# Kernel optimization log

Measured on AMD Instinct MI355X. Metric: run time of the kernel, lower is better.

The kernel has to match this reference:

```python
import jax, jax.numpy as jnp
import numpy as np

N = 50000          # nodes
E = 800000         # edges (avg degree 16)
D = 128            # feature dim
MSG_EPS = 1e-7     # GENConv eps added to relu(msg)
SM_EPS = 1e-16     # pyg softmax denominator eps
BN_EPS = 1e-5
LN_EPS = 1e-5


def setup_inputs() -> dict:
    key = jax.random.key(0)
    ks = jax.random.split(key, 6)
    x = jax.random.normal(ks[0], (N, D), dtype=jnp.float32)
    edge_index = jax.random.randint(ks[1], (2, E), 0, N, dtype=jnp.int32)
    t = jnp.array(1.0, dtype=jnp.float32)
    W1 = jax.random.normal(ks[2], (D, 2 * D), dtype=jnp.float32) / np.sqrt(D).astype(np.float32)
    b1 = jnp.zeros((2 * D,), jnp.float32)
    bn_gamma = jnp.ones((2 * D,), jnp.float32)
    bn_beta = jnp.zeros((2 * D,), jnp.float32)
    W2 = jax.random.normal(ks[3], (2 * D, D), dtype=jnp.float32) / np.sqrt(2 * D).astype(np.float32)
    b2 = jnp.zeros((D,), jnp.float32)
    ln_gamma = jnp.ones((D,), jnp.float32)
    ln_beta = jnp.zeros((D,), jnp.float32)
    return {"x": x, "edge_index": edge_index, "t": t, "W1": W1, "b1": b1,
            "bn_gamma": bn_gamma, "bn_beta": bn_beta, "W2": W2, "b2": b2,
            "ln_gamma": ln_gamma, "ln_beta": ln_beta}


def reference(x, edge_index, t, W1, b1, bn_gamma, bn_beta, W2, b2, ln_gamma, ln_beta):
    src, dst = edge_index[0], edge_index[1]
    # --- GENConv message: relu(x_j) + eps  -> [E, D]
    msg = jax.nn.relu(x[src]) + MSG_EPS
    # --- softmax aggregation over incoming edges per dst node, per feature
    logits = t * msg                                            # [E, D]
    seg_max = jax.ops.segment_max(logits, dst, num_segments=N)  # [N, D]
    seg_max = jnp.where(jnp.isfinite(seg_max), seg_max, 0.0)    # empty segments -> 0
    ex = jnp.exp(logits - seg_max[dst])                         # [E, D]
    denom = jax.ops.segment_sum(ex, dst, num_segments=N)        # [N, D]
    alpha = ex / (denom[dst] + SM_EPS)                          # [E, D]
    agg = jax.ops.segment_sum(alpha * msg, dst, num_segments=N) # [N, D]
    # --- GENConv update: MLP(agg + x), MLP = Lin(D,2D)->BN->ReLU->Lin(2D,D)
    h = agg + x
    h = h @ W1 + b1                                             # [N, 2D]
    mu = jnp.mean(h, axis=0)
    var = jnp.var(h, axis=0)
    h = (h - mu) * jax.lax.rsqrt(var + BN_EPS) * bn_gamma + bn_beta
    h = jax.nn.relu(h)
    h = h @ W2 + b2                                             # [N, D]
    # --- LayerNorm -> ReLU -> (dropout p=0 noop) -> residual
    mu2 = jnp.mean(h, axis=-1, keepdims=True)
    var2 = jnp.mean(jnp.square(h - mu2), axis=-1, keepdims=True)
    h = (h - mu2) * jax.lax.rsqrt(var2 + LN_EPS) * ln_gamma + ln_beta
    h = jax.nn.relu(h)
    return x + h
```

## Files before the change

### kernel.cpp

```cpp
#include <hip/hip_runtime.h>

#define D 128
#define D2 256
#define BSH 5
#define BNODES 32
#define NBMAX 2048
#define CAP 640
#define PCHUNK 4096
#define REP 32
#define CSTRIDE 16
#define ZWORDS (2 * REP * 256 + NBMAX * CSTRIDE)

typedef __attribute__((ext_vector_type(8))) short short8;
typedef __attribute__((ext_vector_type(4))) float f32x4;

__device__ inline unsigned short f2b(float f) {
  unsigned u = __float_as_uint(f);
  unsigned r = (u + 0x7FFFu + ((u >> 16) & 1u)) >> 16;
  return (unsigned short)r;
}
__device__ inline float b2f(unsigned short h) {
  return __uint_as_float(((unsigned)h) << 16);
}
__device__ inline float lo2f(unsigned u) { return __uint_as_float(u << 16); }
__device__ inline float hi2f(unsigned u) { return __uint_as_float(u & 0xffff0000u); }

__global__ __launch_bounds__(256) void prep_kernel(
    const float* __restrict__ x, const float* __restrict__ W1,
    const float* __restrict__ W2, unsigned short* __restrict__ mb,
    unsigned short* __restrict__ W1f, unsigned short* __restrict__ W2f,
    float* __restrict__ zbase, int total4) {
  int idx = blockIdx.x * 256 + threadIdx.x;
  if (idx < 32768) {
    int k = idx >> 8, n = idx & 255;
    int t = n >> 4, m16 = n & 15;
    int kk = k >> 5, quad = (k >> 3) & 3, j = k & 7;
    W1f[(((t * 4 + kk) * 64 + quad * 16 + m16) << 3) + j] = f2b(W1[idx]);
  } else if (idx < 65536) {
    int i = idx - 32768;
    int k = i >> 7, n = i & 127;
    int t = n >> 4, m16 = n & 15;
    int kk = k >> 5, quad = (k >> 3) & 3, j = k & 7;
    W2f[(((t * 8 + kk) * 64 + quad * 16 + m16) << 3) + j] = f2b(W2[i]);
  } else if (idx < 65536 + total4) {
    int i = idx - 65536;
    float4 v = reinterpret_cast<const float4*>(x)[i];
    unsigned lo = (unsigned)f2b(fmaxf(v.x, 0.f) + 1e-7f) |
                  ((unsigned)f2b(fmaxf(v.y, 0.f) + 1e-7f) << 16);
    unsigned hi = (unsigned)f2b(fmaxf(v.z, 0.f) + 1e-7f) |
                  ((unsigned)f2b(fmaxf(v.w, 0.f) + 1e-7f) << 16);
    reinterpret_cast<uint2*>(mb)[i] = make_uint2(lo, hi);
  } else if (idx < 65536 + total4 + 32) {
    reinterpret_cast<uint2*>(mb)[idx - 65536] = make_uint2(0u, 0u);
  } else if (idx < 65536 + total4 + 32 + ZWORDS) {
    zbase[idx - (65536 + total4 + 32)] = 0.f;
  }
}

__global__ __launch_bounds__(256) void part_kernel(const int* __restrict__ ei,
                                                   int* __restrict__ cursor,
                                                   unsigned* __restrict__ pairbuf,
                                                   int E, int nb) {
  __shared__ int cnt[NBMAX];
  __shared__ int base[NBMAX];
  int tid = threadIdx.x;
  int c0 = blockIdx.x * PCHUNK;
  int nE = min(PCHUNK, E - c0);
  for (int i = tid; i < nb; i += 256) cnt[i] = 0;
  __syncthreads();
  for (int j = tid; j < nE; j += 256) {
    int dst = ei[E + c0 + j];
    atomicAdd(&cnt[dst >> BSH], 1);
  }
  __syncthreads();
  for (int i = tid; i < nb; i += 256) {
    int c = cnt[i];
    base[i] = (c > 0) ? atomicAdd(&cursor[i * CSTRIDE], c) : 0;
    cnt[i] = 0;
  }
  __syncthreads();
  for (int j = tid; j < nE; j += 256) {
    int e = c0 + j;
    int dst = ei[E + e];
    int src = ei[e];
    int b = dst >> BSH;
    int r = base[b] + atomicAdd(&cnt[b], 1);
    if (r < CAP)
      pairbuf[(size_t)b * CAP + r] =
          (unsigned)src | ((unsigned)(dst & (BNODES - 1)) << 16);
  }
}

__global__ __launch_bounds__(512) void agg2_kernel(const float* __restrict__ x,
                                                   const unsigned short* __restrict__ mb,
                                                   const unsigned* __restrict__ pairbuf,
                                                   const int* __restrict__ cursor,
                                                   const float* __restrict__ tptr,
                                                   unsigned short* __restrict__ h0b, int N) {
  __shared__ int soff[CAP + 4 * BNODES];
  __shared__ int cnt[BNODES], off[BNODES], run[BNODES], pcnt[BNODES];
  int b = blockIdx.x;
  int tid = threadIdx.x;
  int Eb = min(cursor[b * CSTRIDE], CAP);
  if (tid < BNODES) { cnt[tid] = 0; run[tid] = 0; }
  __syncthreads();
  for (int j = tid; j < Eb; j += 512)
    atomicAdd(&cnt[pairbuf[(size_t)b * CAP + j] >> 16], 1);
  __syncthreads();
  if (tid < BNODES) {
    int c = cnt[tid];
    int pc = (c + 3) & ~3;
    pcnt[tid] = pc;
    int s = pc;
#pragma unroll
    for (int st = 1; st < 32; st <<= 1) {
      int u = __shfl_up(s, st, 32);
      if ((tid & 31) >= st) s += u;
    }
    off[tid] = s - pc;
  }
  __syncthreads();
  for (int j = tid; j < Eb; j += 512) {
    unsigned p = pairbuf[(size_t)b * CAP + j];
    int dl = p >> 16;
    int r = atomicAdd(&run[dl], 1);
    soff[off[dl] + r] = (int)(p & 0xffffu) << 8;
  }
  if (tid < BNODES) {
    int o = off[tid];
    for (int r = cnt[tid]; r < pcnt[tid]; ++r) soff[o + r] = N << 8;
  }
  __syncthreads();

  int w = tid >> 6;
  int l = tid & 63;
  float t = tptr[0];
  int laneoff = l << 2;
  const char* mbase = (const char*)mb;
  for (int ln = w; ln < BNODES; ln += 8) {
    int n = (b << BSH) + ln;
    if (n >= N) continue;
    int s0 = off[ln];
    int dn = pcnt[ln];
    float den0 = 0.f, num0 = 0.f, den1 = 0.f, num1 = 0.f;
    if (dn > 0) {
      unsigned uu[4];
#pragma unroll
      for (int q = 0; q < 4; ++q)
        uu[q] = *(const unsigned*)(mbase + (soff[s0 + q] | laneoff));
      for (int j = 4; j < dn; j += 4) {
        unsigned vv[4];
#pragma unroll
        for (int q = 0; q < 4; ++q)
          vv[q] = *(const unsigned*)(mbase + (soff[s0 + j + q] | laneoff));
#pragma unroll
        for (int q = 0; q < 4; ++q) {
          float m0 = lo2f(uu[q]);
          float m1 = hi2f(uu[q]);
          float e0 = __expf(t * m0);
          float e1 = __expf(t * m1);
          den0 += e0; num0 += e0 * m0;
          den1 += e1; num1 += e1 * m1;
        }
#pragma unroll
        for (int q = 0; q < 4; ++q) uu[q] = vv[q];
      }
#pragma unroll
      for (int q = 0; q < 4; ++q) {
        float m0 = lo2f(uu[q]);
        float m1 = hi2f(uu[q]);
        float e0 = __expf(t * m0);
        float e1 = __expf(t * m1);
        den0 += e0; num0 += e0 * m0;
        den1 += e1; num1 += e1 * m1;
      }
      float fnpad = (float)(dn - cnt[ln]);
      den0 -= fnpad;
      den1 -= fnpad;
    }
    size_t idx = ((size_t)n << 7) + 2 * l;
    float2 xv = *reinterpret_cast<const float2*>(x + idx);
    float v0 = num0 / (den0 + 1e-16f) + xv.x;
    float v1 = num1 / (den1 + 1e-16f) + xv.y;
    *reinterpret_cast<unsigned*>(h0b + idx) =
        (unsigned)f2b(v0) | ((unsigned)f2b(v1) << 16);
  }
}

__global__ __launch_bounds__(256) void gemm1_mfma(
    const unsigned short* __restrict__ h0b, const unsigned short* __restrict__ W1f,
    unsigned short* __restrict__ h1b,
    float* __restrict__ bnsum, float* __restrict__ bnsumsq, int M) {
  __shared__ unsigned short lt[4][64][72];
  int tid = threadIdx.x;
  int w = tid >> 6;
  int l = tid & 63;
  int m16 = l & 15;
  int quad = l >> 4;
  int r0 = blockIdx.x * 64;

  f32x4 acc[4][4];
#pragma unroll
  for (int rt = 0; rt < 4; ++rt)
#pragma unroll
    for (int ct = 0; ct < 4; ++ct) acc[rt][ct] = (f32x4){0.f, 0.f, 0.f, 0.f};

#pragma unroll
  for (int kk = 0; kk < 4; ++kk) {
    short8 bfr[4];
#pragma unroll
    for (int ct = 0; ct < 4; ++ct)
      bfr[ct] = *reinterpret_cast<const short8*>(
          W1f + ((((w * 4 + ct) * 4 + kk) * 64 + l) << 3));
    short8 a[4];
#pragma unroll
    for (int rt = 0; rt < 4; ++rt) {
      int row = min(r0 + rt * 16 + m16, M - 1);
      a[rt] = *reinterpret_cast<const short8*>(h0b + (size_t)row * D + kk * 32 + quad * 8);
    }
#pragma unroll
    for (int rt = 0; rt < 4; ++rt)
#pragma unroll
      for (int ct = 0; ct < 4; ++ct)
        acc[rt][ct] = __builtin_amdgcn_mfma_f32_16x16x32_bf16(a[rt], bfr[ct], acc[rt][ct], 0, 0, 0);
  }

  int rep = (blockIdx.x & (REP - 1)) << 8;
#pragma unroll
  for (int ct = 0; ct < 4; ++ct) {
    int col = w * 64 + ct * 16 + m16;
    float cs = 0.f, cq = 0.f;
#pragma unroll
    for (int rt = 0; rt < 4; ++rt) {
      int rloc = rt * 16 + quad * 4;
#pragma unroll
      for (int reg = 0; reg < 4; ++reg) {
        float val = acc[rt][ct][reg];
        if (r0 + rloc + reg < M) {
          cs += val;
          cq += val * val;
        }
        lt[w][rloc + reg][ct * 16 + m16] = f2b(val);
      }
    }
    cs += __shfl_xor(cs, 16, 64);
    cs += __shfl_xor(cs, 32, 64);
    cq += __shfl_xor(cq, 16, 64);
    cq += __shfl_xor(cq, 32, 64);
    if (quad == 0) {
      atomicAdd(&bnsum[rep + col], cs);
      atomicAdd(&bnsumsq[rep + col], cq);
    }
  }

  int row = r0 + l;
  if (row < M) {
    const unsigned short* src = &lt[w][l][0];
    unsigned short* dst = h1b + (size_t)row * D2 + w * 64;
#pragma unroll
    for (int j = 0; j < 8; ++j)
      *reinterpret_cast<short8*>(dst + j * 8) =
          *reinterpret_cast<const short8*>(src + j * 8);
  }
}

__global__ __launch_bounds__(256) void gemm2_mfma(
    const unsigned short* __restrict__ h1b, const unsigned short* __restrict__ W2f,
    const float* __restrict__ b2, const float* __restrict__ bnsum,
    const float* __restrict__ bnsumsq, const float* __restrict__ bng,
    const float* __restrict__ bnb, const float* __restrict__ lng,
    const float* __restrict__ lnb, const float* __restrict__ x,
    float* __restrict__ out, int M) {
  __shared__ float lnp[64][2], lnp2[64][2];
  __shared__ float sS[D2], sH[D2];
  int tid = threadIdx.x;
  {
    float s = 0.f, q = 0.f;
#pragma unroll
    for (int r = 0; r < REP; ++r) {
      s += bnsum[(r << 8) + tid];
      q += bnsumsq[(r << 8) + tid];
    }
    float invM = 1.f / (float)M;
    float mu = s * invM;
    float var = q * invM - mu * mu;
    float sc = bng[tid] * rsqrtf(var + 1e-5f);
    sS[tid] = sc;
    sH[tid] = bnb[tid] - mu * sc;
  }
  __syncthreads();

  int w = tid >> 6;
  int l = tid & 63;
  int m16 = l & 15;
  int quad = l >> 4;
  int rb = w >> 1, cb = w & 1;
  int r00 = blockIdx.x * 64;

  f32x4 acc[2][4];
#pragma unroll
  for (int rt = 0; rt < 2; ++rt)
#pragma unroll
    for (int ct = 0; ct < 4; ++ct) acc[rt][ct] = (f32x4){0.f, 0.f, 0.f, 0.f};

#pragma unroll
  for (int kk = 0; kk < 8; ++kk) {
    int base = kk * 32 + quad * 8;
    f32x4 s0 = *reinterpret_cast<const f32x4*>(&sS[base]);
    f32x4 s1 = *reinterpret_cast<const f32x4*>(&sS[base + 4]);
    f32x4 g0 = *reinterpret_cast<const f32x4*>(&sH[base]);
    f32x4 g1 = *reinterpret_cast<const f32x4*>(&sH[base + 4]);
    short8 a[2];
#pragma unroll
    for (int rt = 0; rt < 2; ++rt) {
      int row = min(r00 + rb * 32 + rt * 16 + m16, M - 1);
      uint4 raw = *reinterpret_cast<const uint4*>(h1b + (size_t)row * D2 + base);
      unsigned wds[4] = {raw.x, raw.y, raw.z, raw.w};
      unsigned ow[4];
#pragma unroll
      for (int q = 0; q < 4; ++q) {
        f32x4 sv = (q < 2) ? s0 : s1;
        f32x4 gv = (q < 2) ? g0 : g1;
        int e = (q & 1) * 2;
        float v0 = fmaxf(lo2f(wds[q]) * sv[e] + gv[e], 0.f);
        float v1 = fmaxf(hi2f(wds[q]) * sv[e + 1] + gv[e + 1], 0.f);
        ow[q] = (unsigned)f2b(v0) | ((unsigned)f2b(v1) << 16);
      }
      uint4 packed = make_uint4(ow[0], ow[1], ow[2], ow[3]);
      a[rt] = *reinterpret_cast<short8*>(&packed);
    }
    short8 bfr[4];
#pragma unroll
    for (int ct = 0; ct < 4; ++ct)
      bfr[ct] = *reinterpret_cast<const short8*>(
          W2f + ((((cb * 4 + ct) * 8 + kk) * 64 + l) << 3));
#pragma unroll
    for (int rt = 0; rt < 2; ++rt)
#pragma unroll
      for (int ct = 0; ct < 4; ++ct)
        acc[rt][ct] = __builtin_amdgcn_mfma_f32_16x16x32_bf16(a[rt], bfr[ct], acc[rt][ct], 0, 0, 0);
  }

  float b2v[4], lgv[4], lbv[4];
#pragma unroll
  for (int ct = 0; ct < 4; ++ct) {
    int col = cb * 64 + ct * 16 + m16;
    b2v[ct] = b2[col];
    lgv[ct] = lng[col];
    lbv[ct] = lnb[col];
  }

#pragma unroll
  for (int rt = 0; rt < 2; ++rt) {
#pragma unroll
    for (int reg = 0; reg < 4; ++reg) {
      float s = 0.f, s2 = 0.f;
#pragma unroll
      for (int ct = 0; ct < 4; ++ct) {
        float v = acc[rt][ct][reg] + b2v[ct];
        s += v;
        s2 += v * v;
      }
#pragma unroll
      for (int msk = 1; msk < 16; msk <<= 1) {
        s += __shfl_xor(s, msk, 64);
        s2 += __shfl_xor(s2, msk, 64);
      }
      if (m16 == 0) {
        int rl = rb * 32 + rt * 16 + quad * 4 + reg;
        lnp[rl][cb] = s;
        lnp2[rl][cb] = s2;
      }
    }
  }
  __syncthreads();

#pragma unroll
  for (int rt = 0; rt < 2; ++rt) {
#pragma unroll
    for (int reg = 0; reg < 4; ++reg) {
      int rl = rb * 32 + rt * 16 + quad * 4 + reg;
      int row = r00 + rl;
      float s = lnp[rl][0] + lnp[rl][1];
      float s2 = lnp2[rl][0] + lnp2[rl][1];
      float mu = s * (1.f / 128.f);
      float var = s2 * (1.f / 128.f) - mu * mu;
      float inv = rsqrtf(var + 1e-5f);
      if (row < M) {
#pragma unroll
        for (int ct = 0; ct < 4; ++ct) {
          int col = cb * 64 + ct * 16 + m16;
          float v = acc[rt][ct][reg] + b2v[ct];
          float h = fmaxf((v - mu) * inv * lgv[ct] + lbv[ct], 0.f);
          out[(size_t)row * D + col] = x[(size_t)row * D + col] + h;
        }
      }
    }
  }
}

extern "C" void kernel_launch(void* const* d_in, const int* in_sizes, int n_in,
                              void* d_out, int out_size, void* d_ws, size_t ws_size,
                              hipStream_t stream) {
  const float* x   = (const float*)d_in[0];
  const int*   ei  = (const int*)d_in[1];
  const float* t   = (const float*)d_in[2];
  const float* W1  = (const float*)d_in[3];
  const float* bng = (const float*)d_in[5];
  const float* bnb = (const float*)d_in[6];
  const float* W2  = (const float*)d_in[7];
  const float* b2  = (const float*)d_in[8];
  const float* lng = (const float*)d_in[9];
  const float* lnb = (const float*)d_in[10];
  float* out = (float*)d_out;

  int N = in_sizes[0] / D;
  int E = in_sizes[1] / 2;
  size_t nd = (size_t)N * D;
  int nb = (N + BNODES - 1) >> BSH;

  unsigned short* mb  = (unsigned short*)d_ws;
  unsigned short* h0b = mb + nd + 128;
  unsigned short* h1b = h0b + nd;
  unsigned short* W1f = h1b + 2 * nd;
  unsigned short* W2f = W1f + 32768;
  float* bnsum   = (float*)(W2f + 32768);
  float* bnsumsq = bnsum + REP * 256;
  int* cursor    = (int*)(bnsumsq + REP * 256);
  unsigned* pairbuf = (unsigned*)(cursor + NBMAX * CSTRIDE);

  int total4 = (int)(nd / 4);
  int ptotal = 65536 + total4 + 32 + ZWORDS;
  prep_kernel<<<(ptotal + 255) / 256, 256, 0, stream>>>(x, W1, W2, mb, W1f, W2f,
                                                        bnsum, total4);

  part_kernel<<<(E + PCHUNK - 1) / PCHUNK, 256, 0, stream>>>(ei, cursor, pairbuf, E, nb);
  agg2_kernel<<<nb, 512, 0, stream>>>(x, mb, pairbuf, cursor, t, h0b, N);

  gemm1_mfma<<<(N + 63) / 64, 256, 0, stream>>>(h0b, W1f, h1b, bnsum, bnsumsq, N);
  gemm2_mfma<<<(N + 63) / 64, 256, 0, stream>>>(h1b, W2f, b2, bnsum, bnsumsq,
                                                bng, bnb, lng, lnb, x, out, N);
}
```

Baseline: 207.9 us.

## Widen aggregation gathers to 16-byte rows and prescale messages for native exp2

The aggregation kernel now has each 16-lane quarter-wave load a full 256-byte bf16 row with uint4 loads, so one wave handles four edges at once instead of 4-byte per-lane gathers. Partial sums are combined with cross-lane shuffles, and only the first quarter writes the output. Messages are prescaled by t*log2(e) in the prep kernel so the inner loop can use raw v_exp_f32 (exp2) without a multiply, and the numerator is rescaled by ln2/t at the end. This cuts gather instruction count and exp arithmetic, at the cost of extra shuffles, more accumulator registers, and a small added bf16 rounding difference from prescaling.

```diff
diff --git a/kernel.cpp b/kernel.cpp
--- a/kernel.cpp
+++ b/kernel.cpp
@@ -19,15 +19,13 @@
   unsigned r = (u + 0x7FFFu + ((u >> 16) & 1u)) >> 16;
   return (unsigned short)r;
 }
-__device__ inline float b2f(unsigned short h) {
-  return __uint_as_float(((unsigned)h) << 16);
-}
 __device__ inline float lo2f(unsigned u) { return __uint_as_float(u << 16); }
 __device__ inline float hi2f(unsigned u) { return __uint_as_float(u & 0xffff0000u); }
 
 __global__ __launch_bounds__(256) void prep_kernel(
     const float* __restrict__ x, const float* __restrict__ W1,
-    const float* __restrict__ W2, unsigned short* __restrict__ mb,
+    const float* __restrict__ W2, const float* __restrict__ tptr,
+    unsigned short* __restrict__ mb,
     unsigned short* __restrict__ W1f, unsigned short* __restrict__ W2f,
     float* __restrict__ zbase, int total4) {
   int idx = blockIdx.x * 256 + threadIdx.x;
@@ -44,11 +42,12 @@
     W2f[(((t * 8 + kk) * 64 + quad * 16 + m16) << 3) + j] = f2b(W2[i]);
   } else if (idx < 65536 + total4) {
     int i = idx - 65536;
+    float scl = tptr[0] * 1.4426950408889634f;
     float4 v = reinterpret_cast<const float4*>(x)[i];
-    unsigned lo = (unsigned)f2b(fmaxf(v.x, 0.f) + 1e-7f) |
-                  ((unsigned)f2b(fmaxf(v.y, 0.f) + 1e-7f) << 16);
-    unsigned hi = (unsigned)f2b(fmaxf(v.z, 0.f) + 1e-7f) |
-                  ((unsigned)f2b(fmaxf(v.w, 0.f) + 1e-7f) << 16);
+    unsigned lo = (unsigned)f2b(scl * (fmaxf(v.x, 0.f) + 1e-7f)) |
+                  ((unsigned)f2b(scl * (fmaxf(v.y, 0.f) + 1e-7f)) << 16);
+    unsigned hi = (unsigned)f2b(scl * (fmaxf(v.z, 0.f) + 1e-7f)) |
+                  ((unsigned)f2b(scl * (fmaxf(v.w, 0.f) + 1e-7f)) << 16);
     reinterpret_cast<uint2*>(mb)[i] = make_uint2(lo, hi);
   } else if (idx < 65536 + total4 + 32) {
     reinterpret_cast<uint2*>(mb)[idx - 65536] = make_uint2(0u, 0u);
@@ -134,57 +133,81 @@
 
   int w = tid >> 6;
   int l = tid & 63;
-  float t = tptr[0];
-  int laneoff = l << 2;
+  int q = l >> 4;
+  int li = l & 15;
+  float tval = tptr[0];
+  float numscale = 0.69314718055994531f / tval;
+  int laneoff = li << 4;
   const char* mbase = (const char*)mb;
+
+#define LDROW(JG) \
+  (*reinterpret_cast<const uint4*>(mbase + (soff[s0 + ((JG) << 2) + q] | laneoff)))
+#define PROC(W)                                                     \
+  do {                                                              \
+    unsigned _w0 = (W).x, _w1 = (W).y, _w2 = (W).z, _w3 = (W).w;    \
+    unsigned _ws[4] = {_w0, _w1, _w2, _w3};                         \
+    _Pragma("unroll")                                               \
+    for (int k = 0; k < 4; ++k) {                                   \
+      float u0 = lo2f(_ws[k]);                                      \
+      float u1 = hi2f(_ws[k]);                                      \
+      float e0, e1;                                                 \
+      asm("v_exp_f32 %0, %1" : "=v"(e0) : "v"(u0));                 \
+      asm("v_exp_f32 %0, %1" : "=v"(e1) : "v"(u1));                 \
+      den[2 * k] += e0;                                             \
+      num[2 * k] = fmaf(e0, u0, num[2 * k]);                        \
+      den[2 * k + 1] += e1;                                         \
+      num[2 * k + 1] = fmaf(e1, u1, num[2 * k + 1]);                \
+    }                                                               \
+  } while (0)
+
   for (int ln = w; ln < BNODES; ln += 8) {
     int n = (b << BSH) + ln;
     if (n >= N) continue;
     int s0 = off[ln];
     int dn = pcnt[ln];
-    float den0 = 0.f, num0 = 0.f, den1 = 0.f, num1 = 0.f;
+    float den[8] = {0.f, 0.f, 0.f, 0.f, 0.f, 0.f, 0.f, 0.f};
+    float num[8] = {0.f, 0.f, 0.f, 0.f, 0.f, 0.f, 0.f, 0.f};
     if (dn > 0) {
-      unsigned uu[4];
-#pragma unroll
-      for (int q = 0; q < 4; ++q)
-        uu[q] = *(const unsigned*)(mbase + (soff[s0 + q] | laneoff));
-      for (int j = 4; j < dn; j += 4) {
-        unsigned vv[4];
-#pragma unroll
-        for (int q = 0; q < 4; ++q)
-          vv[q] = *(const unsigned*)(mbase + (soff[s0 + j + q] | laneoff));
-#pragma unroll
-        for (int q = 0; q < 4; ++q) {
-          float m0 = lo2f(uu[q]);
-          float m1 = hi2f(uu[q]);
-          float e0 = __expf(t * m0);
-          float e1 = __expf(t * m1);
-          den0 += e0; num0 += e0 * m0;
-          den1 += e1; num1 += e1 * m1;
-        }
-#pragma unroll
-        for (int q = 0; q < 4; ++q) uu[q] = vv[q];
-      }
-#pragma unroll
-      for (int q = 0; q < 4; ++q) {
-        float m0 = lo2f(uu[q]);
-        float m1 = hi2f(uu[q]);
-        float e0 = __expf(t * m0);
-        float e1 = __expf(t * m1);
-        den0 += e0; num0 += e0 * m0;
-        den1 += e1; num1 += e1 * m1;
+      int g = dn >> 2;
+      uint4 uu = LDROW(0);
+      uint4 vv = uu;
+      if (g > 1) vv = LDROW(1);
+      for (int jg = 2; jg < g; ++jg) {
+        uint4 ww = LDROW(jg);
+        PROC(uu);
+        uu = vv;
+        vv = ww;
+      }
+      PROC(uu);
+      if (g > 1) PROC(vv);
+#pragma unroll
+      for (int k = 0; k < 8; ++k) {
+        den[k] += __shfl_xor(den[k], 16, 64);
+        den[k] += __shfl_xor(den[k], 32, 64);
+        num[k] += __shfl_xor(num[k], 16, 64);
+        num[k] += __shfl_xor(num[k], 32, 64);
       }
       float fnpad = (float)(dn - cnt[ln]);
-      den0 -= fnpad;
-      den1 -= fnpad;
-    }
-    size_t idx = ((size_t)n << 7) + 2 * l;
-    float2 xv = *reinterpret_cast<const float2*>(x + idx);
-    float v0 = num0 / (den0 + 1e-16f) + xv.x;
-    float v1 = num1 / (den1 + 1e-16f) + xv.y;
-    *reinterpret_cast<unsigned*>(h0b + idx) =
-        (unsigned)f2b(v0) | ((unsigned)f2b(v1) << 16);
-  }
+#pragma unroll
+      for (int k = 0; k < 8; ++k) den[k] -= fnpad;
+    }
+    if (q == 0) {
+      size_t idx = ((size_t)n << 7) + (li << 3);
+      float4 xa = *reinterpret_cast<const float4*>(x + idx);
+      float4 xb = *reinterpret_cast<const float4*>(x + idx + 4);
+      float xs[8] = {xa.x, xa.y, xa.z, xa.w, xb.x, xb.y, xb.z, xb.w};
+      unsigned ow[4];
+#pragma unroll
+      for (int k = 0; k < 4; ++k) {
+        float v0 = num[2 * k] * numscale / (den[2 * k] + 1e-16f) + xs[2 * k];
+        float v1 = num[2 * k + 1] * numscale / (den[2 * k + 1] + 1e-16f) + xs[2 * k + 1];
+        ow[k] = (unsigned)f2b(v0) | ((unsigned)f2b(v1) << 16);
+      }
+      *reinterpret_cast<uint4*>(h0b + idx) = make_uint4(ow[0], ow[1], ow[2], ow[3]);
+    }
+  }
+#undef LDROW
+#undef PROC
 }
 
 __global__ __launch_bounds__(256) void gemm1_mfma(
@@ -431,7 +454,7 @@
 
   int total4 = (int)(nd / 4);
   int ptotal = 65536 + total4 + 32 + ZWORDS;
-  prep_kernel<<<(ptotal + 255) / 256, 256, 0, stream>>>(x, W1, W2, mb, W1f, W2f,
+  prep_kernel<<<(ptotal + 255) / 256, 256, 0, stream>>>(x, W1, W2, t, mb, W1f, W2f,
                                                         bnsum, total4);
 
   part_kernel<<<(E + PCHUNK - 1) / PCHUNK, 256, 0, stream>>>(ei, cursor, pairbuf, E, nb);
```

After: 220.9 us. 6.2% more time.
